# Kernel tuning notes

Measured on AMD Instinct MI355X. Metric: run time of the kernel, lower is better.

## Reference

```python
import jax, jax.numpy as jnp
import numpy as np

B, N, IN_DIM, OUT_DIM, H = 4, 2048, 256, 256, 8
ATN = OUT_DIM // H  # 32


def setup_inputs() -> dict:
    key = jax.random.key(0)
    k1, k2, k3, k4, k5 = jax.random.split(key, 5)
    x = jax.random.normal(k1, (B, N, IN_DIM), dtype=jnp.float32)
    adj = jax.random.uniform(k2, (B, N, N), dtype=jnp.float32)
    # stacked per-head Linear weights/biases and bilinear corelation matrices
    W = jax.random.normal(k3, (H, IN_DIM, ATN), dtype=jnp.float32) / np.sqrt(IN_DIM)
    b = jax.random.normal(k4, (H, ATN), dtype=jnp.float32) * 0.01
    C = jax.random.normal(k5, (H, ATN, ATN), dtype=jnp.float32) / np.sqrt(ATN)
    return {"x": x, "adj": adj, "W": W, "b": b, "C": C}


def reference(x, adj, W, b, C):
    # x: [B,N,in_dim]; adj: [B,N,N]; W: [H,in_dim,atn]; b: [H,atn]; C: [H,atn,atn]
    # per-head linear projection -> [B,H,N,atn]
    xt = jnp.einsum('bni,hio->bhno', x, W) + b[None, :, None, :]
    # bilinear scores: (xt @ C^T) @ xt^T ; torch einsum 'akj,ij->aki' contracts
    # the second index of corelation, i.e. xC = xt @ C.T
    xC = jnp.einsum('bhno,hpo->bhnp', xt, C)          # [B,H,N,atn]
    scores = jnp.einsum('bhnp,bhmp->bhnm', xC, xt)    # [B,H,N,N]
    alpha = jnp.tanh(scores * adj[:, None, :, :])     # mask then tanh
    heads = jnp.einsum('bhnm,bhmo->bhno', alpha, xt)  # [B,H,N,atn]
    # concat heads on feature dim -> [B,N,H*atn]
    out = jnp.transpose(heads, (0, 2, 1, 3)).reshape(x.shape[0], x.shape[1], -1)
    return out
```

## Files before the change

### kernel.cpp

```cpp
#include <hip/hip_runtime.h>
#include <hip/hip_bf16.h>


typedef __bf16 bf16;
typedef __attribute__((ext_vector_type(8))) __bf16 bf16x8;
typedef __attribute__((ext_vector_type(4))) __bf16 bf16x4;
typedef __attribute__((ext_vector_type(4))) float  f32x4;

#define MFMA(a, b, c) __builtin_amdgcn_mfma_f32_16x16x32_bf16(a, b, c, 0, 0, 0)

#define GLDS16(g, l) __builtin_amdgcn_global_load_lds(                        \
        (const __attribute__((address_space(1))) void*)(g),                   \
        (__attribute__((address_space(3))) void*)(l), 16, 0, 0)

#define WAITVM10() __builtin_amdgcn_s_waitcnt(0x0F7A)
#define WAITVM8()  __builtin_amdgcn_s_waitcnt(0x0F78)
#define FENCE()    __builtin_amdgcn_sched_barrier(0)
#define BAR()      __builtin_amdgcn_s_barrier()

__device__ __forceinline__ float fast_tanh(float x) {
    float e = __builtin_amdgcn_exp2f(x * 2.88539008177792681f);
    float r = __builtin_amdgcn_rcpf(e + 1.0f);
    return __builtin_fmaf(-2.0f, r, 1.0f);
}

#define BB   4
#define NN   2048
#define IND  256
#define HH   8
#define ATN  32

#define OFF_XBF   0u
#define OFF_XT    4194304u
#define OFF_XC    8388608u
#define OFF_XTT   12582912u
#define OFF_WT    16777216u
#define OFF_CB    16908288u
#define OFF_SLAB  16924672u

__global__ __launch_bounds__(256) void k_prep(const float* __restrict__ x,
                                              const float* __restrict__ W,
                                              const float* __restrict__ C,
                                              bf16* __restrict__ xbf,
                                              bf16* __restrict__ WT,
                                              bf16* __restrict__ Cb) {
    int tid = blockIdx.x * 256 + threadIdx.x;
    if (tid < 524288) {
        float4 v = ((const float4*)x)[tid];
        bf16x4 o;
        o[0] = (bf16)v.x; o[1] = (bf16)v.y; o[2] = (bf16)v.z; o[3] = (bf16)v.w;
        *(bf16x4*)(xbf + (size_t)tid * 4) = o;
    } else if (tid < 524288 + 65536) {
        int t = tid - 524288;
        int h = t >> 13, r = t & 8191, i = r >> 5, o = r & 31;
        WT[(h * 32 + o) * 256 + i] = (bf16)W[t];
    } else if (tid < 524288 + 65536 + 8192) {
        int t = tid - (524288 + 65536);
        Cb[t] = (bf16)C[t];
    }
}

__global__ __launch_bounds__(256) void k_proj(const bf16* __restrict__ xbf,
                                              const bf16* __restrict__ WT,
                                              const bf16* __restrict__ Cb,
                                              const float* __restrict__ bias,
                                              bf16* __restrict__ xt,
                                              bf16* __restrict__ xc,
                                              bf16* __restrict__ xtT) {
    __shared__ bf16 ldsA_all[4][32 * 40];
    __shared__ bf16 ldsB_all[4][32 * 40];
    int bid = blockIdx.x;
    int ntg = bid & 15, h = (bid >> 4) & 7, b = bid >> 7;
    int wave = threadIdx.x >> 6;
    int lane = threadIdx.x & 63;
    int nt = ntg * 4 + wave;
    int n0 = nt * 32;
    int c = lane & 15, q = lane >> 4;
    bf16* ldsA = ldsA_all[wave];
    bf16* ldsB = ldsB_all[wave];

    f32x4 acc[2][2] = {};
    const bf16* xrow0 = xbf + ((size_t)(b * NN + n0 + c) * IND + q * 8);
    const bf16* xrow1 = xbf + ((size_t)(b * NN + n0 + 16 + c) * IND + q * 8);
    const bf16* wrow0 = WT + ((h * 32 + c) * IND + q * 8);
    const bf16* wrow1 = WT + ((h * 32 + 16 + c) * IND + q * 8);
#pragma unroll
    for (int k0 = 0; k0 < IND; k0 += 32) {
        bf16x8 a0 = *(const bf16x8*)(xrow0 + k0);
        bf16x8 a1 = *(const bf16x8*)(xrow1 + k0);
        bf16x8 w0 = *(const bf16x8*)(wrow0 + k0);
        bf16x8 w1 = *(const bf16x8*)(wrow1 + k0);
        acc[0][0] = MFMA(a0, w0, acc[0][0]);
        acc[0][1] = MFMA(a0, w1, acc[0][1]);
        acc[1][0] = MFMA(a1, w0, acc[1][0]);
        acc[1][1] = MFMA(a1, w1, acc[1][1]);
    }
    float bv[2] = { bias[h * 32 + c], bias[h * 32 + 16 + c] };
    size_t bh = (size_t)(b * HH + h);
#pragma unroll
    for (int nq = 0; nq < 2; ++nq)
#pragma unroll
        for (int oq = 0; oq < 2; ++oq)
#pragma unroll
            for (int r = 0; r < 4; ++r)
                ldsA[(nq * 16 + q * 4 + r) * 40 + oq * 16 + c] =
                    (bf16)(acc[nq][oq][r] + bv[oq]);
    f32x4 acc2[2][2] = {};
    bf16x8 aL0 = *(const bf16x8*)(ldsA + (c) * 40 + q * 8);
    bf16x8 aL1 = *(const bf16x8*)(ldsA + (16 + c) * 40 + q * 8);
    bf16x8 c0 = *(const bf16x8*)(Cb + h * 1024 + (c) * 32 + q * 8);
    bf16x8 c1 = *(const bf16x8*)(Cb + h * 1024 + (16 + c) * 32 + q * 8);
    acc2[0][0] = MFMA(aL0, c0, acc2[0][0]);
    acc2[0][1] = MFMA(aL0, c1, acc2[0][1]);
    acc2[1][0] = MFMA(aL1, c0, acc2[1][0]);
    acc2[1][1] = MFMA(aL1, c1, acc2[1][1]);
#pragma unroll
    for (int nq = 0; nq < 2; ++nq)
#pragma unroll
        for (int pq = 0; pq < 2; ++pq)
#pragma unroll
            for (int r = 0; r < 4; ++r)
                ldsB[(nq * 16 + q * 4 + r) * 40 + pq * 16 + c] =
                    (bf16)acc2[nq][pq][r];

    {
        int n = lane >> 1, half = lane & 1;
        bf16x8 t0 = *(const bf16x8*)(ldsA + n * 40 + half * 16);
        bf16x8 t1 = *(const bf16x8*)(ldsA + n * 40 + half * 16 + 8);
        bf16* dst = xt + (bh * NN + n0 + n) * ATN + half * 16;
        *(bf16x8*)(dst) = t0;
        *(bf16x8*)(dst + 8) = t1;
        bf16x8 u0 = *(const bf16x8*)(ldsB + n * 40 + half * 16);
        bf16x8 u1 = *(const bf16x8*)(ldsB + n * 40 + half * 16 + 8);
        bf16* dst2 = xc + (bh * NN + n0 + n) * ATN + half * 16;
        *(bf16x8*)(dst2) = u0;
        *(bf16x8*)(dst2 + 8) = u1;
    }
    {
        int o = lane >> 1, nh = lane & 1;
        bf16x8 t0, t1;
#pragma unroll
        for (int i = 0; i < 8; ++i) {
            t0[i] = ldsA[(nh * 16 + i) * 40 + o];
            t1[i] = ldsA[(nh * 16 + 8 + i) * 40 + o];
        }
        bf16* dst = xtT + (bh * ATN + o) * NN + n0 + nh * 16;
        *(bf16x8*)(dst) = t0;
        *(bf16x8*)(dst + 8) = t1;
    }
}

__global__ __launch_bounds__(512, 4) void k_attn(const float* __restrict__ adj,
                                                 const bf16* __restrict__ xt,
                                                 const bf16* __restrict__ xc,
                                                 const bf16* __restrict__ xtT,
                                                 bf16* __restrict__ sl0,
                                                 bf16* __restrict__ sl1,
                                                 bf16* __restrict__ sl2,
                                                 float* __restrict__ out) {
    __shared__ float adjlds[6 * 1024];
    int bid = blockIdx.x;
    int chunk = bid >> 8;
    int bn = bid & 255;
    int nt = bn & 63, b = bn >> 6;
    int n0 = nt * 32;
    int wave = threadIdx.x >> 6;
    int lane = threadIdx.x & 63;
    int c = lane & 15, q = lane >> 4;
    int p = 8 * (c >> 2) + (c & 3);
    size_t bh = (size_t)(b * HH + wave);
    const bf16* xt_h = xt + bh * NN * ATN;
    const bf16* xc_h = xc + bh * NN * ATN;
    const bf16* xtT_h = xtT + bh * ATN * NN;
    const float* adj_b = adj + (size_t)b * NN * NN;
    const int m_beg = chunk * 512;

    int nloc = wave * 8 + (lane >> 3);
    int gsub = (lane & 7) ^ (lane >> 3);
    const float* gA = adj_b + (size_t)(n0 + nloc) * NN + gsub * 4 + m_beg;

#define DMA(t) do { if (wave < 4)                                              \
        GLDS16(gA + (t) * 32, adjlds + ((t) % 6) * 1024 + wave * 256);         \
    } while (0)

    bf16x8 bXC0 = *(const bf16x8*)(xc_h + (n0 + c) * ATN + q * 8);
    bf16x8 bXC1 = *(const bf16x8*)(xc_h + (n0 + 16 + c) * ATN + q * 8);
    f32x4 accO[2][2] = {};
    const f32x4 z = {0.f, 0.f, 0.f, 0.f};

    bf16x8 xA0e, xA1e, oA0e, oA1e, xA0o, xA1o, oA0o, oA1o;
#define REGS_E(t) do { int m0 = m_beg + (t) * 32;                              \
        xA0e = *(const bf16x8*)(xt_h + (size_t)(m0 + p) * ATN + q * 8);        \
        xA1e = *(const bf16x8*)(xt_h + (size_t)(m0 + p + 4) * ATN + q * 8);    \
        oA0e = *(const bf16x8*)(xtT_h + (size_t)(c) * NN + m0 + q * 8);        \
        oA1e = *(const bf16x8*)(xtT_h + (size_t)(16 + c) * NN + m0 + q * 8);   \
    } while (0)
#define REGS_O(t) do { int m0 = m_beg + (t) * 32;                              \
        xA0o = *(const bf16x8*)(xt_h + (size_t)(m0 + p) * ATN + q * 8);        \
        xA1o = *(const bf16x8*)(xt_h + (size_t)(m0 + p + 4) * ATN + q * 8);    \
        oA0o = *(const bf16x8*)(xtT_h + (size_t)(c) * NN + m0 + q * 8);        \
        oA1o = *(const bf16x8*)(xtT_h + (size_t)(16 + c) * NN + m0 + q * 8);   \
    } while (0)

    int ad00 = c * 32 + ((2 * q) ^ (c & 7)) * 4;
    int ad01 = c * 32 + ((2 * q + 1) ^ (c & 7)) * 4;
    int ad10 = (16 + c) * 32 + ((2 * q) ^ (c & 7)) * 4;
    int ad11 = (16 + c) * 32 + ((2 * q + 1) ^ (c & 7)) * 4;

#define COMPUTE(t, xA0, xA1, oA0, oA1) do {                                    \
        const float* lb = adjlds + ((t) % 6) * 1024;                           \
        f32x4 A00 = *(const f32x4*)(lb + ad00);                                \
        f32x4 A01 = *(const f32x4*)(lb + ad01);                                \
        f32x4 A10 = *(const f32x4*)(lb + ad10);                                \
        f32x4 A11 = *(const f32x4*)(lb + ad11);                                \
        f32x4 S0a = MFMA(xA0, bXC0, z);             \
        f32x4 S0b = MFMA(xA1, bXC0, z);             \
        f32x4 S1a = MFMA(xA0, bXC1, z);             \
        f32x4 S1b = MFMA(xA1, bXC1, z);                                        \
        bf16x8 P0, P1;                                                         \
        _Pragma("unroll") for (int r = 0; r < 4; ++r) {                        \
            P0[r]     = (bf16)fast_tanh(S0a[r] * A00[r]);                      \
            P0[4 + r] = (bf16)fast_tanh(S0b[r] * A01[r]);                      \
            P1[r]     = (bf16)fast_tanh(S1a[r] * A10[r]);                      \
            P1[4 + r] = (bf16)fast_tanh(S1b[r] * A11[r]);                      \
        }                                                                      \
        accO[0][0] = MFMA(oA0, P0, accO[0][0]);                                \
        accO[0][1] = MFMA(oA0, P1, accO[0][1]);                                \
        accO[1][0] = MFMA(oA1, P0, accO[1][0]);                                \
        accO[1][1] = MFMA(oA1, P1, accO[1][1]);                                \
    } while (0)

    DMA(0); DMA(1); DMA(2); DMA(3);
    REGS_E(0); REGS_O(1);
#pragma unroll
    for (int tt = 0; tt <= 12; tt += 2) {
        FENCE(); WAITVM10(); BAR(); FENCE();
        if (tt + 4 < 16) { DMA(tt + 4); DMA(tt + 5); }
        COMPUTE(tt,     xA0e, xA1e, oA0e, oA1e);
        COMPUTE(tt + 1, xA0o, xA1o, oA0o, oA1o);
        FENCE();
        REGS_E(tt + 2); REGS_O(tt + 3);
    }
    FENCE(); WAITVM8(); BAR(); FENCE();
    COMPUTE(14, xA0e, xA1e, oA0e, oA1e);
    COMPUTE(15, xA0o, xA1o, oA0o, oA1o);

#undef DMA
#undef REGS_E
#undef REGS_O
#undef COMPUTE

    if (chunk == 3) {
#pragma unroll
        for (int oq = 0; oq < 2; ++oq)
#pragma unroll
            for (int nq = 0; nq < 2; ++nq) {
                size_t n = n0 + nq * 16 + c;
                *(f32x4*)&out[((size_t)b * NN + n) * 256 + wave * 32 + oq * 16 + 4 * q] =
                    accO[oq][nq];
            }
    } else {
        bf16* sl = (chunk == 0) ? sl0 : (chunk == 1 ? sl1 : sl2);
#pragma unroll
        for (int oq = 0; oq < 2; ++oq)
#pragma unroll
            for (int nq = 0; nq < 2; ++nq) {
                size_t n = n0 + nq * 16 + c;
                bf16x4 v;
#pragma unroll
                for (int r = 0; r < 4; ++r) v[r] = (bf16)accO[oq][nq][r];
                *(bf16x4*)&sl[((size_t)b * NN + n) * 256 + wave * 32 + oq * 16 + 4 * q] = v;
            }
    }
}

__global__ __launch_bounds__(256) void k_reduce(const bf16* __restrict__ sl0,
                                                const bf16* __restrict__ sl1,
                                                const bf16* __restrict__ sl2,
                                                float* __restrict__ out) {
    int i = blockIdx.x * 256 + threadIdx.x;
    f32x4 a = ((const f32x4*)out)[i];
    bf16x4 s0 = ((const bf16x4*)sl0)[i];
    bf16x4 s1 = ((const bf16x4*)sl1)[i];
    bf16x4 s2 = ((const bf16x4*)sl2)[i];
#pragma unroll
    for (int r = 0; r < 4; ++r)
        a[r] += (float)s0[r] + (float)s1[r] + (float)s2[r];
    ((f32x4*)out)[i] = a;
}

extern "C" void kernel_launch(void* const* d_in, const int* in_sizes, int n_in,
                              void* d_out, int out_size, void* d_ws, size_t ws_size,
                              hipStream_t stream) {
    const float* x    = (const float*)d_in[0];
    const float* adj  = (const float*)d_in[1];
    const float* W    = (const float*)d_in[2];
    const float* bias = (const float*)d_in[3];
    const float* C    = (const float*)d_in[4];
    float* out = (float*)d_out;

    char* ws = (char*)d_ws;
    bf16*  xbf  = (bf16*)(ws + OFF_XBF);
    bf16*  xt   = (bf16*)(ws + OFF_XT);
    bf16*  xc   = (bf16*)(ws + OFF_XC);
    bf16*  xtT  = (bf16*)(ws + OFF_XTT);
    bf16*  WT   = (bf16*)(ws + OFF_WT);
    bf16*  Cb   = (bf16*)(ws + OFF_CB);
    bf16*  sl0  = (bf16*)(ws + OFF_XBF);
    bf16*  sl1  = (bf16*)(ws + OFF_SLAB);
    bf16*  sl2  = (bf16*)(ws + OFF_SLAB + 4194304u);

    k_prep<<<2336, 256, 0, stream>>>(x, W, C, xbf, WT, Cb);
    k_proj<<<512, 256, 0, stream>>>(xbf, WT, Cb, bias, xt, xc, xtT);
    k_attn<<<1024, 512, 0, stream>>>(adj, xt, xc, xtT, sl0, sl1, sl2, out);
    k_reduce<<<2048, 256, 0, stream>>>(sl0, sl1, sl2, out);
}
```

Baseline: 168.7 us.

## Replace split-K partial slabs and reduce kernel with atomic float accumulation

The attention kernel's four key-range chunks now accumulate straight into the fp32 output with atomicAdd. The output is zeroed in the prep kernel. This drops the bf16 partial-slab writes and the separate reduce launch, and also keeps fp32 precision for the partials. Block indexing is remapped so the chunks and batches for one row tile are launched close together, which may help L2 locality. In exchange there are many scalar float atomics, each element touched by four chunks, which could contend and adds nondeterministic summation order.

```diff
diff --git a/kernel.cpp b/kernel.cpp
--- a/kernel.cpp
+++ b/kernel.cpp
@@ -36,14 +36,14 @@
 #define OFF_XTT   12582912u
 #define OFF_WT    16777216u
 #define OFF_CB    16908288u
-#define OFF_SLAB  16924672u
 
 __global__ __launch_bounds__(256) void k_prep(const float* __restrict__ x,
                                               const float* __restrict__ W,
                                               const float* __restrict__ C,
                                               bf16* __restrict__ xbf,
                                               bf16* __restrict__ WT,
-                                              bf16* __restrict__ Cb) {
+                                              bf16* __restrict__ Cb,
+                                              float* __restrict__ out) {
     int tid = blockIdx.x * 256 + threadIdx.x;
     if (tid < 524288) {
         float4 v = ((const float4*)x)[tid];
@@ -57,6 +57,10 @@
     } else if (tid < 524288 + 65536 + 8192) {
         int t = tid - (524288 + 65536);
         Cb[t] = (bf16)C[t];
+    } else if (tid >= 598016) {
+        int t = tid - 598016;
+        float4 zz = {0.f, 0.f, 0.f, 0.f};
+        ((float4*)out)[t] = zz;
     }
 }
 
@@ -154,15 +158,13 @@
                                                  const bf16* __restrict__ xt,
                                                  const bf16* __restrict__ xc,
                                                  const bf16* __restrict__ xtT,
-                                                 bf16* __restrict__ sl0,
-                                                 bf16* __restrict__ sl1,
-                                                 bf16* __restrict__ sl2,
                                                  float* __restrict__ out) {
     __shared__ float adjlds[6 * 1024];
-    int bid = blockIdx.x;
-    int chunk = bid >> 8;
-    int bn = bid & 255;
-    int nt = bn & 63, b = bn >> 6;
+    int L = blockIdx.x;
+    int g = L & 15;
+    int j = L >> 4;
+    int chunk = g >> 2, b = g & 3;
+    int nt = j;
     int n0 = nt * 32;
     int wave = threadIdx.x >> 6;
     int lane = threadIdx.x & 63;
@@ -250,43 +252,16 @@
 #undef REGS_O
 #undef COMPUTE
 
-    if (chunk == 3) {
-#pragma unroll
-        for (int oq = 0; oq < 2; ++oq)
-#pragma unroll
-            for (int nq = 0; nq < 2; ++nq) {
-                size_t n = n0 + nq * 16 + c;
-                *(f32x4*)&out[((size_t)b * NN + n) * 256 + wave * 32 + oq * 16 + 4 * q] =
-                    accO[oq][nq];
-            }
-    } else {
-        bf16* sl = (chunk == 0) ? sl0 : (chunk == 1 ? sl1 : sl2);
-#pragma unroll
-        for (int oq = 0; oq < 2; ++oq)
-#pragma unroll
-            for (int nq = 0; nq < 2; ++nq) {
-                size_t n = n0 + nq * 16 + c;
-                bf16x4 v;
-#pragma unroll
-                for (int r = 0; r < 4; ++r) v[r] = (bf16)accO[oq][nq][r];
-                *(bf16x4*)&sl[((size_t)b * NN + n) * 256 + wave * 32 + oq * 16 + 4 * q] = v;
-            }
-    }
-}
-
-__global__ __launch_bounds__(256) void k_reduce(const bf16* __restrict__ sl0,
-                                                const bf16* __restrict__ sl1,
-                                                const bf16* __restrict__ sl2,
-                                                float* __restrict__ out) {
-    int i = blockIdx.x * 256 + threadIdx.x;
-    f32x4 a = ((const f32x4*)out)[i];
-    bf16x4 s0 = ((const bf16x4*)sl0)[i];
-    bf16x4 s1 = ((const bf16x4*)sl1)[i];
-    bf16x4 s2 = ((const bf16x4*)sl2)[i];
-#pragma unroll
-    for (int r = 0; r < 4; ++r)
-        a[r] += (float)s0[r] + (float)s1[r] + (float)s2[r];
-    ((f32x4*)out)[i] = a;
+#pragma unroll
+    for (int oq = 0; oq < 2; ++oq)
+#pragma unroll
+        for (int nq = 0; nq < 2; ++nq) {
+            size_t n = n0 + nq * 16 + c;
+            float* pr = &out[((size_t)b * NN + n) * 256 + wave * 32 + oq * 16 + 4 * q];
+#pragma unroll
+            for (int r = 0; r < 4; ++r)
+                atomicAdd(pr + r, accO[oq][nq][r]);
+        }
 }
 
 extern "C" void kernel_launch(void* const* d_in, const int* in_sizes, int n_in,
@@ -306,12 +281,8 @@
     bf16*  xtT  = (bf16*)(ws + OFF_XTT);
     bf16*  WT   = (bf16*)(ws + OFF_WT);
     bf16*  Cb   = (bf16*)(ws + OFF_CB);
-    bf16*  sl0  = (bf16*)(ws + OFF_XBF);
-    bf16*  sl1  = (bf16*)(ws + OFF_SLAB);
-    bf16*  sl2  = (bf16*)(ws + OFF_SLAB + 4194304u);
-
-    k_prep<<<2336, 256, 0, stream>>>(x, W, C, xbf, WT, Cb);
+
+    k_prep<<<4384, 256, 0, stream>>>(x, W, C, xbf, WT, Cb, out);
     k_proj<<<512, 256, 0, stream>>>(xbf, WT, Cb, bias, xt, xc, xtT);
-    k_attn<<<1024, 512, 0, stream>>>(adj, xt, xc, xtT, sl0, sl1, sl2, out);
-    k_reduce<<<2048, 256, 0, stream>>>(sl0, sl1, sl2, out);
-}
+    k_attn<<<1024, 512, 0, stream>>>(adj, xt, xc, xtT, out);
+}
```

Result: slower. 243.7 us (+44.4%).
